# Kernel optimization log

Measured on AMD Instinct MI355X. Metric: run time of the kernel, lower is better.

Reference implementation:

```python
import jax, jax.numpy as jnp
import numpy as np

N_JOBS, N_MACH = 30, 20
N = N_JOBS * N_MACH          # 600 nodes
IN_DIM = 2
H = 128                      # hidden_dim_feature_extractor
HA = 256                     # hidden_dim_actor
HC = 256                     # hidden_dim_critic
E = 9600                     # edges
BN_EPS = 1e-5


def setup_inputs() -> dict:
    key = jax.random.key(0)
    ks = jax.random.split(key, 16)
    init = lambda k, shp: (jax.random.normal(k, shp, jnp.float32) * 0.05)
    d = {
        "features": jax.random.normal(ks[0], (N, IN_DIM), jnp.float32),
        "edge_index": jax.random.randint(ks[1], (2, E), 0, N, jnp.int32),
        # GIN layer 0 MLP: Linear(IN,H) -> BN -> ReLU -> Linear(H,H)
        "g0_W0": init(ks[2], (IN_DIM, H)), "g0_b0": jnp.zeros((H,), jnp.float32),
        "g0_gamma": jnp.ones((H,), jnp.float32), "g0_beta": jnp.zeros((H,), jnp.float32),
        "g0_W1": init(ks[3], (H, H)), "g0_b1": jnp.zeros((H,), jnp.float32),
        # GIN layer 1 MLP: Linear(H,H) -> BN -> ReLU -> Linear(H,H)
        "g1_W0": init(ks[4], (H, H)), "g1_b0": jnp.zeros((H,), jnp.float32),
        "g1_gamma": jnp.ones((H,), jnp.float32), "g1_beta": jnp.zeros((H,), jnp.float32),
        "g1_W1": init(ks[5], (H, H)), "g1_b1": jnp.zeros((H,), jnp.float32),
        # actor MLP: Linear(3H,HA) -> ReLU -> Linear(HA,1)
        "a_W0": init(ks[6], (3 * H, HA)), "a_b0": jnp.zeros((HA,), jnp.float32),
        "a_W1": init(ks[7], (HA, 1)), "a_b1": jnp.zeros((1,), jnp.float32),
        # critic MLP: Linear(H,HC) -> ReLU -> Linear(HC,1)
        "c_W0": init(ks[8], (H, HC)), "c_b0": jnp.zeros((HC,), jnp.float32),
        "c_W1": init(ks[9], (HC, 1)), "c_b1": jnp.zeros((1,), jnp.float32),
    }
    return d


def _gin_mlp(h, W0, b0, gamma, beta, W1, b1):
    # Linear -> BatchNorm(train-mode batch stats) -> ReLU -> Linear
    h1 = h @ W0 + b0
    mu = h1.mean(axis=0)
    var = h1.var(axis=0)
    h1 = gamma * (h1 - mu) * jax.lax.rsqrt(var + BN_EPS) + beta
    return jax.nn.relu(h1) @ W1 + b1


def reference(features, edge_index,
              g0_W0, g0_b0, g0_gamma, g0_beta, g0_W1, g0_b1,
              g1_W0, g1_b0, g1_gamma, g1_beta, g1_W1, g1_b1,
              a_W0, a_b0, a_W1, a_b1,
              c_W0, c_b0, c_W1, c_b1):
    src, dst = edge_index[0], edge_index[1]

    def gin(x, *mlp_params):
        # GINConv with eps=0: MLP(x + sum_{j in N(i)} x_j)
        agg = jax.ops.segment_sum(x[src], dst, num_segments=N)
        return _gin_mlp(x + agg, *mlp_params)

    h = gin(features, g0_W0, g0_b0, g0_gamma, g0_beta, g0_W1, g0_b1)
    h = gin(h, g1_W0, g1_b0, g1_gamma, g1_beta, g1_W1, g1_b1)   # (N, H)

    # graph pooling: (ones/N) @ h  == mean over nodes
    ge = h.mean(axis=0, keepdims=True)                           # (1, H)
    value = jax.nn.relu(ge @ c_W0 + c_b0) @ c_W1 + c_b1          # (1, 1)

    # s_a_pairs row k (k = i*N + j): [ge, h[j] (tile), h[i] (repeat_interleave)]
    # Fuse concat + first actor matmul by splitting a_W0 into three H-blocks.
    Ws, Wn1, Wn2 = a_W0[:H], a_W0[H:2 * H], a_W0[2 * H:]
    pre = (ge @ Ws + a_b0)[None, :, :] + (h @ Wn1)[None, :, :] + (h @ Wn2)[:, None, :]
    logits = jax.nn.relu(pre).reshape(N * N, HA) @ a_W1 + a_b1   # (N^2, 1)
    pi = jax.nn.softmax(logits, axis=0)
    return pi, value
```

## Files before the change

### kernel.cpp

```cpp
#include <hip/hip_runtime.h>
#include <math.h>

#define N_NODES 600
#define N_EDGES 9600
#define HDIM    128
#define HA      256
#define NN      360000
#define BN_EPS  1e-5f
#define NTILE   361

#define OFF_U     0
#define OFF_BAB   1200
#define OFF_SUMZ  1456
#define OFF_SUMZ2 1584
#define OFF_R1SUM 1712
#define OFF_MAXA  1840
#define OFF_SUMA  2352
#define OFF_CSR   2864
#define OFF_WC1   13072
#define OFF_WC2   45840
#define OFF_H0    78608
#define OFF_Z     155408
#define OFF_A     232208
#define OFF_B     385808

typedef _Float16 h2 __attribute__((ext_vector_type(2)));
typedef _Float16 h4 __attribute__((ext_vector_type(4)));
typedef _Float16 h8 __attribute__((ext_vector_type(8)));

__device__ __forceinline__ float dot2acc(h2 a, h2 b, float c) {
#if __has_builtin(__builtin_amdgcn_fdot2)
  return __builtin_amdgcn_fdot2(a, b, c, false);
#else
  return c + (float)a.x * (float)b.x + (float)a.y * (float)b.y;
#endif
}

__device__ __forceinline__ h2 relu2(h2 x) {
  h2 z = {(_Float16)0, (_Float16)0};
#if __has_builtin(__builtin_elementwise_max)
  return __builtin_elementwise_max(x, z);
#else
  h2 r;
  r.x = x.x > z.x ? x.x : z.x;
  r.y = x.y > z.y ? x.y : z.y;
  return r;
#endif
}

__device__ __forceinline__ h4 toh4(float4 v) {
  h4 r;
  r.x = (_Float16)v.x; r.y = (_Float16)v.y;
  r.z = (_Float16)v.z; r.w = (_Float16)v.w;
  return r;
}

struct KP {
  const float* feat; const int* ei;
  const float *g0W0, *g0ga, *g0be, *g0W1, *g0b1;
  const float *g1W0, *g1ga, *g1be, *g1W1, *g1b1;
  const float *aW0, *ab0, *aW1;
  const float *cW0, *cb0, *cW1, *cb1;
  float* ws; float* out;
};

__global__ __launch_bounds__(256) void k_indep(KP p) {
  __shared__ float sm[1536];
  const int b = blockIdx.x, t = threadIdx.x;

  if (b < 25) {
    float* us = sm;
    if (t < 48) us[t] = 0.f;
    __syncthreads();
    const int lo = b * 24, hi = lo + 24;
    for (int e = t; e < N_EDGES; e += 256) {
      int d = p.ei[N_EDGES + e];
      if (d >= lo && d < hi) {
        int s = p.ei[e];
        atomicAdd(&us[2 * (d - lo)],     p.feat[2 * s]);
        atomicAdd(&us[2 * (d - lo) + 1], p.feat[2 * s + 1]);
      }
    }
    __syncthreads();
    if (t < 48) p.ws[OFF_U + b * 48 + t] = us[t] + p.feat[b * 48 + t];
  } else if (b == 25) {
    int* si = (int*)sm;
    int* cnt = si; int* bs = si + 600; int* off = si + 856;
    int* rs_g = (int*)(p.ws + OFF_CSR);
    int* src_g = rs_g + 604;
    for (int i = t; i < 600; i += 256) cnt[i] = 0;
    __syncthreads();
    for (int e = t; e < N_EDGES; e += 256) atomicAdd(&cnt[p.ei[N_EDGES + e]], 1);
    __syncthreads();
    int lsum = 0;
    if (t < 200) lsum = cnt[3 * t] + cnt[3 * t + 1] + cnt[3 * t + 2];
    bs[t] = lsum; __syncthreads();
    for (int d = 1; d < 256; d <<= 1) {
      int v = (t >= d) ? bs[t - d] : 0;
      __syncthreads();
      bs[t] += v;
      __syncthreads();
    }
    if (t < 200) {
      int base = bs[t] - lsum;
      off[3 * t] = base;
      off[3 * t + 1] = base + cnt[3 * t];
      off[3 * t + 2] = base + cnt[3 * t] + cnt[3 * t + 1];
    }
    if (t == 0) off[600] = N_EDGES;
    __syncthreads();
    for (int i = t; i < 601; i += 256) rs_g[i] = off[i];
    for (int i = t; i < 600; i += 256) cnt[i] = off[i];
    __syncthreads();
    for (int e = t; e < N_EDGES; e += 256) {
      int d = p.ei[N_EDGES + e];
      int pos = atomicAdd(&cnt[d], 1);
      src_g[pos] = p.ei[e];
    }
  } else if (b < 90) {
    int o = (b - 26) * 1024 + t * 4;
    int mat = o >> 15, rem = o & 32767;
    int j = rem >> 8, k = rem & 255;
    const float* aw = p.aW0 + (HDIM + mat * HDIM) * HA + k;
    float4 acc = make_float4(0, 0, 0, 0);
#pragma unroll 8
    for (int m = 0; m < HDIM; m++) {
      float w = p.g1W1[j * HDIM + m];
      const float4 v = *(const float4*)(aw + m * HA);
      acc.x += w * v.x; acc.y += w * v.y; acc.z += w * v.z; acc.w += w * v.w;
    }
    *(float4*)(p.ws + (mat ? OFF_WC2 : OFF_WC1) + j * HA + k) = acc;
  } else {
    float acc = 0.f;
#pragma unroll 8
    for (int m = 0; m < HDIM; m++)
      acc += p.g1b1[m] * (p.aW0[(HDIM + m) * HA + t] + p.aW0[(2 * HDIM + m) * HA + t]);
    p.ws[OFF_BAB + t] = acc;
    if (t < 128) {
      p.ws[OFF_SUMZ + t] = 0.f;
      p.ws[OFF_SUMZ2 + t] = 0.f;
      p.ws[OFF_R1SUM + t] = 0.f;
    }
  }
}

__global__ __launch_bounds__(256) void k_l0(KP p) {
  __shared__ float ua[1200];
  __shared__ float bn[384];
  __shared__ float r0s[512];
  __shared__ float wred[24];
  const int b = blockIdx.x, t = threadIdx.x;
  for (int i = t; i < 1200; i += 256) ua[i] = p.ws[OFF_U + i];
  __syncthreads();
  float s0 = 0, s1 = 0, s00 = 0, s11 = 0, s01 = 0;
  for (int n = t; n < N_NODES; n += 256) {
    float u0 = ua[2 * n], u1 = ua[2 * n + 1];
    s0 += u0; s1 += u1; s00 += u0 * u0; s11 += u1 * u1; s01 += u0 * u1;
  }
#pragma unroll
  for (int off = 32; off > 0; off >>= 1) {
    s0  += __shfl_xor(s0, off);  s1  += __shfl_xor(s1, off);
    s00 += __shfl_xor(s00, off); s11 += __shfl_xor(s11, off);
    s01 += __shfl_xor(s01, off);
  }
  const int wv = t >> 6, ln = t & 63;
  if (ln == 0) {
    wred[wv * 5 + 0] = s0;  wred[wv * 5 + 1] = s1;  wred[wv * 5 + 2] = s00;
    wred[wv * 5 + 3] = s11; wred[wv * 5 + 4] = s01;
  }
  __syncthreads();
  if (t < HDIM) {
    float tot[5];
#pragma unroll
    for (int q = 0; q < 5; q++)
      tot[q] = wred[q] + wred[5 + q] + wred[10 + q] + wred[15 + q];
    float m0 = tot[0] / 600.f, m1 = tot[1] / 600.f;
    float v00 = tot[2] / 600.f - m0 * m0;
    float v11 = tot[3] / 600.f - m1 * m1;
    float v01 = tot[4] / 600.f - m0 * m1;
    float W00 = p.g0W0[t], W01 = p.g0W0[HDIM + t];
    float var = W00 * W00 * v00 + W01 * W01 * v11 + 2.f * W00 * W01 * v01;
    float sc = p.g0ga[t] * rsqrtf(var + BN_EPS);
    float mu = m0 * W00 + m1 * W01;
    bn[t] = sc * W00; bn[128 + t] = sc * W01; bn[256 + t] = p.g0be[t] - mu * sc;
  }
  __syncthreads();
  const int n0 = b * 4;
#pragma unroll
  for (int pq = 0; pq < 2; pq++) {
    int idx = pq * 256 + t, n = idx >> 7, j = idx & 127;
    float u0 = ua[2 * (n0 + n)], u1 = ua[2 * (n0 + n) + 1];
    r0s[n * 128 + j] = fmaxf(u0 * bn[j] + u1 * bn[128 + j] + bn[256 + j], 0.f);
  }
  __syncthreads();
#pragma unroll
  for (int pq = 0; pq < 2; pq++) {
    int idx = pq * 256 + t, n = idx >> 7, c = idx & 127;
    const float* row = r0s + n * 128;
    float acc = p.g0b1[c];
#pragma unroll 8
    for (int j = 0; j < HDIM; j++) acc += row[j] * p.g0W1[j * HDIM + c];
    p.ws[OFF_H0 + (n0 + n) * HDIM + c] = acc;
  }
}

__global__ __launch_bounds__(256) void k_zstats(KP p) {
  __shared__ float t1[4 * 128];
  __shared__ float red[256];
  const int b = blockIdx.x, t = threadIdx.x, n0 = b * 4;
  const int* rs = (const int*)(p.ws + OFF_CSR);
  const int* srcv = rs + 604;
  const float* h0 = p.ws + OFF_H0;
#pragma unroll
  for (int pq = 0; pq < 2; pq++) {
    int idx = pq * 256 + t, n = idx >> 7, c = idx & 127;
    int node = n0 + n;
    float v = h0[node * HDIM + c];
    int e0 = rs[node], e1 = rs[node + 1];
    for (int e = e0; e < e1; e++) v += h0[srcv[e] * HDIM + c];
    t1[n * 128 + c] = v;
  }
  __syncthreads();
  float zs = 0.f, zs2 = 0.f;
#pragma unroll
  for (int pq = 0; pq < 2; pq++) {
    int idx = pq * 256 + t, n = idx >> 7, c = idx & 127;
    const float* row = t1 + n * 128;
    float acc = 0.f;
#pragma unroll 8
    for (int j = 0; j < HDIM; j++) acc += row[j] * p.g1W0[j * HDIM + c];
    p.ws[OFF_Z + (n0 + n) * HDIM + c] = acc;
    zs += acc; zs2 += acc * acc;
  }
  red[t] = zs; __syncthreads();
  if (t < 128) atomicAdd(&p.ws[OFF_SUMZ + t], red[t] + red[t + 128]);
  __syncthreads();
  red[t] = zs2; __syncthreads();
  if (t < 128) atomicAdd(&p.ws[OFF_SUMZ2 + t], red[t] + red[t + 128]);
}

__global__ __launch_bounds__(256) void k_rab(KP p) {
  __shared__ float r1[4 * 128];
  __shared__ float scl[128], shf[128];
  const int b = blockIdx.x, t = threadIdx.x, n0 = b * 4;
  if (t < 128) {
    float mu = p.ws[OFF_SUMZ + t] * (1.f / 600.f);
    float var = p.ws[OFF_SUMZ2 + t] * (1.f / 600.f) - mu * mu;
    float sc = p.g1ga[t] * rsqrtf(var + BN_EPS);
    scl[t] = sc; shf[t] = p.g1be[t] - mu * sc;
  }
  __syncthreads();
#pragma unroll
  for (int pq = 0; pq < 2; pq++) {
    int idx = pq * 256 + t, n = idx >> 7, j = idx & 127;
    float z = p.ws[OFF_Z + (n0 + n) * HDIM + j];
    r1[n * 128 + j] = fmaxf(z * scl[j] + shf[j], 0.f);
  }
  __syncthreads();
  if (t < 128)
    atomicAdd(&p.ws[OFF_R1SUM + t], r1[t] + r1[128 + t] + r1[256 + t] + r1[384 + t]);
  const float* wc1 = p.ws + OFF_WC1;
  const float* wc2 = p.ws + OFF_WC2;
  float a0 = 0, a1 = 0, a2 = 0, a3 = 0, b0 = 0, b1 = 0, b2 = 0, b3 = 0;
#pragma unroll 4
  for (int j = 0; j < HDIM; j++) {
    float w1 = wc1[j * HA + t], w2 = wc2[j * HA + t];
    float r0v = r1[j], r1v = r1[128 + j], r2v = r1[256 + j], r3v = r1[384 + j];
    a0 += r0v * w1; a1 += r1v * w1; a2 += r2v * w1; a3 += r3v * w1;
    b0 += r0v * w2; b1 += r1v * w2; b2 += r2v * w2; b3 += r3v * w2;
  }
  float* A = p.ws + OFF_A; float* Bm = p.ws + OFF_B;
  A[n0 * HA + t] = a0; A[(n0 + 1) * HA + t] = a1;
  A[(n0 + 2) * HA + t] = a2; A[(n0 + 3) * HA + t] = a3;
  Bm[n0 * HA + t] = b0; Bm[(n0 + 1) * HA + t] = b1;
  Bm[(n0 + 2) * HA + t] = b2; Bm[(n0 + 3) * HA + t] = b3;
}

__global__ __launch_bounds__(256) void k_heads(KP p) {
  __shared__ h4 AsL[2048];
  __shared__ h4 BsL[2048];
  __shared__ h4 wlp[64];
  __shared__ h4 hsp[64];
  __shared__ float ge[128];
  __shared__ float geh[128];
  __shared__ float hsge[256];
  __shared__ float red[256];
  const int b = blockIdx.x, t = threadIdx.x;

  if (t < 128) ge[t] = p.ws[OFF_R1SUM + t] * (1.f / 600.f);
  __syncthreads();
  if (t < 128) {
    float acc = p.g1b1[t];
#pragma unroll 8
    for (int j = 0; j < HDIM; j++) acc += ge[j] * p.g1W1[j * HDIM + t];
    geh[t] = acc;
  }
  __syncthreads();
  {
    float acc = p.ab0[t] + p.ws[OFF_BAB + t];
#pragma unroll 8
    for (int c = 0; c < HDIM; c++) acc += geh[c] * p.aW0[c * HA + t];
    hsge[t] = acc;
  }
  if (b == 0) {
    float v = p.cb0[t];
#pragma unroll 8
    for (int c = 0; c < HDIM; c++) v += geh[c] * p.cW0[c * HA + t];
    v = fmaxf(v, 0.f);
    red[t] = v * p.cW1[t];
    __syncthreads();
    for (int off = 128; off > 0; off >>= 1) {
      if (t < off) red[t] += red[t + off];
      __syncthreads();
    }
    if (t == 0) p.out[NN] = red[0] + p.cb1[0];
  }
  __syncthreads();
  if (t < 64) {
    wlp[t] = toh4(*(const float4*)(p.aW1 + 4 * t));
    hsp[t] = toh4(*(const float4*)(hsge + 4 * t));
  }
  __syncthreads();

  const int tj = b % 19, ti = b / 19;
  const int j0 = tj * 32, i0 = ti * 32;
  const float* A  = p.ws + OFF_A;
  const float* Bm = p.ws + OFF_B;
#pragma unroll
  for (int q = 0; q < 8; q++) {
    int f = q * 256 + t;
    int r = f >> 6;
    int c4 = f & 63;
    int k = c4 * 4;
    int sw = c4 * 32 + (r ^ (c4 & 30));
    float4 av = (j0 + r < N_NODES) ? *(const float4*)(A + (j0 + r) * HA + k)
                                   : make_float4(0, 0, 0, 0);
    AsL[sw] = toh4(av) + hsp[c4];
    float4 bv = (i0 + r < N_NODES) ? *(const float4*)(Bm + (i0 + r) * HA + k)
                                   : make_float4(0, 0, 0, 0);
    BsL[sw] = toh4(bv);
  }
  __syncthreads();

  const int tx = t & 15, ty = t >> 4;
  const int jl = tx * 2, il = ty * 2;
  float a00 = 0, a01 = 0, a10 = 0, a11 = 0;
#pragma unroll 8
  for (int kk2 = 0; kk2 < 64; kk2++) {
    int s = kk2 & 30;
    h8 va = *(h8*)&AsL[kk2 * 32 + (jl ^ s)];
    h8 vb = *(h8*)&BsL[kk2 * 32 + (il ^ s)];
    h4 vw = wlp[kk2];
    h2 wlo = __builtin_shufflevector(vw, vw, 0, 1);
    h2 whi = __builtin_shufflevector(vw, vw, 2, 3);
    h2 aj0lo = __builtin_shufflevector(va, va, 0, 1);
    h2 aj0hi = __builtin_shufflevector(va, va, 2, 3);
    h2 aj1lo = __builtin_shufflevector(va, va, 4, 5);
    h2 aj1hi = __builtin_shufflevector(va, va, 6, 7);
    h2 bi0lo = __builtin_shufflevector(vb, vb, 0, 1);
    h2 bi0hi = __builtin_shufflevector(vb, vb, 2, 3);
    h2 bi1lo = __builtin_shufflevector(vb, vb, 4, 5);
    h2 bi1hi = __builtin_shufflevector(vb, vb, 6, 7);
    a00 = dot2acc(relu2(aj0lo + bi0lo), wlo, a00);
    a00 = dot2acc(relu2(aj0hi + bi0hi), whi, a00);
    a01 = dot2acc(relu2(aj1lo + bi0lo), wlo, a01);
    a01 = dot2acc(relu2(aj1hi + bi0hi), whi, a01);
    a10 = dot2acc(relu2(aj0lo + bi1lo), wlo, a10);
    a10 = dot2acc(relu2(aj0hi + bi1hi), whi, a10);
    a11 = dot2acc(relu2(aj1lo + bi1lo), wlo, a11);
    a11 = dot2acc(relu2(aj1hi + bi1hi), whi, a11);
  }

  const int gi = i0 + il, gj = j0 + jl;
  const bool vi0 = gi < N_NODES, vi1 = gi + 1 < N_NODES;
  const bool vj0 = gj < N_NODES, vj1 = gj + 1 < N_NODES;
  float m = -INFINITY;
  if (vi0 && vj0) m = fmaxf(m, a00);
  if (vi0 && vj1) m = fmaxf(m, a01);
  if (vi1 && vj0) m = fmaxf(m, a10);
  if (vi1 && vj1) m = fmaxf(m, a11);
  __syncthreads();
  red[t] = m;
  __syncthreads();
  for (int off = 128; off > 0; off >>= 1) {
    if (t < off) red[t] = fmaxf(red[t], red[t + off]);
    __syncthreads();
  }
  const float mb = red[0];
  float s = 0.f;
  if (vi0 && vj0) { float e = expf(a00 - mb); p.out[gi * N_NODES + gj] = e; s += e; }
  if (vi0 && vj1) { float e = expf(a01 - mb); p.out[gi * N_NODES + gj + 1] = e; s += e; }
  if (vi1 && vj0) { float e = expf(a10 - mb); p.out[(gi + 1) * N_NODES + gj] = e; s += e; }
  if (vi1 && vj1) { float e = expf(a11 - mb); p.out[(gi + 1) * N_NODES + gj + 1] = e; s += e; }
  __syncthreads();
  red[t] = s;
  __syncthreads();
  for (int off = 128; off > 0; off >>= 1) {
    if (t < off) red[t] += red[t + off];
    __syncthreads();
  }
  if (t == 0) { p.ws[OFF_MAXA + b] = mb; p.ws[OFF_SUMA + b] = red[0]; }
}

__global__ __launch_bounds__(256) void k_fin(KP p) {
  __shared__ float red[256];
  __shared__ float sc19[19];
  const int b = blockIdx.x, t = threadIdx.x;
  const float* maxa = p.ws + OFF_MAXA;
  const float* suma = p.ws + OFF_SUMA;
  float m = -INFINITY;
  if (t < NTILE) m = maxa[t];
  if (t + 256 < NTILE) m = fmaxf(m, maxa[t + 256]);
  red[t] = m;
  __syncthreads();
  for (int off = 128; off > 0; off >>= 1) {
    if (t < off) red[t] = fmaxf(red[t], red[t + off]);
    __syncthreads();
  }
  const float gmax = red[0];
  __syncthreads();
  float s = 0.f;
  if (t < NTILE) s += suma[t] * expf(maxa[t] - gmax);
  if (t + 256 < NTILE) s += suma[t + 256] * expf(maxa[t + 256] - gmax);
  red[t] = s;
  __syncthreads();
  for (int off = 128; off > 0; off >>= 1) {
    if (t < off) red[t] += red[t + off];
    __syncthreads();
  }
  const float invtot = 1.0f / red[0];
  const int ti = b >> 5;
  if (t < 19) sc19[t] = expf(maxa[ti * 19 + t] - gmax) * invtot;
  __syncthreads();
  if (t < 150) {
    float4 v = *(const float4*)(p.out + b * N_NODES + 4 * t);
    float sc = sc19[(4 * t) >> 5];
    v.x *= sc; v.y *= sc; v.z *= sc; v.w *= sc;
    *(float4*)(p.out + b * N_NODES + 4 * t) = v;
  }
}

extern "C" void kernel_launch(void* const* d_in, const int* in_sizes, int n_in,
                              void* d_out, int out_size, void* d_ws, size_t ws_size,
                              hipStream_t stream) {
  KP p;
  p.feat = (const float*)d_in[0];
  p.ei   = (const int*)  d_in[1];
  p.g0W0 = (const float*)d_in[2];
  p.g0ga = (const float*)d_in[4];  p.g0be = (const float*)d_in[5];
  p.g0W1 = (const float*)d_in[6];  p.g0b1 = (const float*)d_in[7];
  p.g1W0 = (const float*)d_in[8];
  p.g1ga = (const float*)d_in[10]; p.g1be = (const float*)d_in[11];
  p.g1W1 = (const float*)d_in[12]; p.g1b1 = (const float*)d_in[13];
  p.aW0  = (const float*)d_in[14]; p.ab0  = (const float*)d_in[15];
  p.aW1  = (const float*)d_in[16];
  p.cW0  = (const float*)d_in[18]; p.cb0  = (const float*)d_in[19];
  p.cW1  = (const float*)d_in[20]; p.cb1  = (const float*)d_in[21];
  p.ws   = (float*)d_ws;
  p.out  = (float*)d_out;

  k_indep <<<91,    256, 0, stream>>>(p);
  k_l0    <<<150,   256, 0, stream>>>(p);
  k_zstats<<<150,   256, 0, stream>>>(p);
  k_rab   <<<150,   256, 0, stream>>>(p);
  k_heads <<<NTILE, 256, 0, stream>>>(p);
  k_fin   <<<600,   256, 0, stream>>>(p);
}
```

Baseline: 93.34 us.

## Fold GIN layer-0 output linear into layer-1 weights and fuse kernels

Result: faster. 79.75 us (-14.6%).

```diff
diff --git a/kernel.cpp b/kernel.cpp
--- a/kernel.cpp
+++ b/kernel.cpp
@@ -5,24 +5,28 @@
 #define N_EDGES 9600
 #define HDIM    128
 #define HA      256
+#define HC      256
 #define NN      360000
 #define BN_EPS  1e-5f
 #define NTILE   361
 
-#define OFF_U     0
-#define OFF_BAB   1200
-#define OFF_SUMZ  1456
-#define OFF_SUMZ2 1584
-#define OFF_R1SUM 1712
-#define OFF_MAXA  1840
-#define OFF_SUMA  2352
-#define OFF_CSR   2864
-#define OFF_WC1   13072
-#define OFF_WC2   45840
-#define OFF_H0    78608
-#define OFF_Z     155408
-#define OFF_A     232208
-#define OFF_B     385808
+#define OFF_U      0
+#define OFF_BCONST 1200
+#define OFF_BF     1456
+#define OFF_SUMZ   1584
+#define OFF_SUMZ2  1712
+#define OFF_R1SUM  1840
+#define OFF_RACC   1968
+#define OFF_MAXA   2224
+#define OFF_SUMA   2736
+#define OFF_CSR    3248
+#define OFF_WF     13456
+#define OFF_WC1    29840
+#define OFF_WC2    62608
+#define OFF_WGS    95376
+#define OFF_Z      128144
+#define OFF_A      204944
+#define OFF_B      358544
 
 typedef _Float16 h2 __attribute__((ext_vector_type(2)));
 typedef _Float16 h4 __attribute__((ext_vector_type(4)));
@@ -117,11 +121,12 @@
       int pos = atomicAdd(&cnt[d], 1);
       src_g[pos] = p.ei[e];
     }
-  } else if (b < 90) {
+  } else if (b < 122) {
     int o = (b - 26) * 1024 + t * 4;
     int mat = o >> 15, rem = o & 32767;
     int j = rem >> 8, k = rem & 255;
-    const float* aw = p.aW0 + (HDIM + mat * HDIM) * HA + k;
+    int rowbase = (mat == 0) ? HDIM : (mat == 1 ? 2 * HDIM : 0);
+    const float* aw = p.aW0 + rowbase * HA + k;
     float4 acc = make_float4(0, 0, 0, 0);
 #pragma unroll 8
     for (int m = 0; m < HDIM; m++) {
@@ -129,14 +134,34 @@
       const float4 v = *(const float4*)(aw + m * HA);
       acc.x += w * v.x; acc.y += w * v.y; acc.z += w * v.z; acc.w += w * v.w;
     }
-    *(float4*)(p.ws + (mat ? OFF_WC2 : OFF_WC1) + j * HA + k) = acc;
+    int dst = (mat == 0) ? OFF_WC1 : (mat == 1 ? OFF_WC2 : OFF_WGS);
+    *(float4*)(p.ws + dst + j * HA + k) = acc;
+  } else if (b < 138) {
+    int o = (b - 122) * 1024 + t * 4;
+    int j = o >> 7, c = o & 127;
+    float4 acc = make_float4(0, 0, 0, 0);
+#pragma unroll 8
+    for (int m = 0; m < HDIM; m++) {
+      float w = p.g0W1[j * HDIM + m];
+      const float4 v = *(const float4*)(p.g1W0 + m * HDIM + c);
+      acc.x += w * v.x; acc.y += w * v.y; acc.z += w * v.z; acc.w += w * v.w;
+    }
+    *(float4*)(p.ws + OFF_WF + j * HDIM + c) = acc;
   } else {
     float acc = 0.f;
 #pragma unroll 8
-    for (int m = 0; m < HDIM; m++)
-      acc += p.g1b1[m] * (p.aW0[(HDIM + m) * HA + t] + p.aW0[(2 * HDIM + m) * HA + t]);
-    p.ws[OFF_BAB + t] = acc;
+    for (int m = 0; m < HDIM; m++) {
+      float gb = p.g1b1[m];
+      acc += gb * (p.aW0[m * HA + t] + p.aW0[(HDIM + m) * HA + t] +
+                   p.aW0[(2 * HDIM + m) * HA + t]);
+    }
+    p.ws[OFF_BCONST + t] = p.ab0[t] + acc;
+    p.ws[OFF_RACC + t] = 0.f;
     if (t < 128) {
+      float a2 = 0.f;
+#pragma unroll 8
+      for (int m = 0; m < HDIM; m++) a2 += p.g0b1[m] * p.g1W0[m * HDIM + t];
+      p.ws[OFF_BF + t] = a2;
       p.ws[OFF_SUMZ + t] = 0.f;
       p.ws[OFF_SUMZ2 + t] = 0.f;
       p.ws[OFF_R1SUM + t] = 0.f;
@@ -144,17 +169,19 @@
   }
 }
 
-__global__ __launch_bounds__(256) void k_l0(KP p) {
-  __shared__ float ua[1200];
+__global__ __launch_bounds__(256) void k_zagg(KP p) {
+  __shared__ float2 u2[600];
   __shared__ float bn[384];
-  __shared__ float r0s[512];
+  __shared__ float r0agg[512];
+  __shared__ float red[256];
   __shared__ float wred[24];
-  const int b = blockIdx.x, t = threadIdx.x;
-  for (int i = t; i < 1200; i += 256) ua[i] = p.ws[OFF_U + i];
+  const int b = blockIdx.x, t = threadIdx.x, n0 = b * 4;
+  const float2* ug = (const float2*)(p.ws + OFF_U);
+  for (int i = t; i < 600; i += 256) u2[i] = ug[i];
   __syncthreads();
   float s0 = 0, s1 = 0, s00 = 0, s11 = 0, s01 = 0;
   for (int n = t; n < N_NODES; n += 256) {
-    float u0 = ua[2 * n], u1 = ua[2 * n + 1];
+    float u0 = u2[n].x, u1 = u2[n].y;
     s0 += u0; s1 += u1; s00 += u0 * u0; s11 += u1 * u1; s01 += u0 * u1;
   }
 #pragma unroll
@@ -185,51 +212,34 @@
     bn[t] = sc * W00; bn[128 + t] = sc * W01; bn[256 + t] = p.g0be[t] - mu * sc;
   }
   __syncthreads();
-  const int n0 = b * 4;
-#pragma unroll
-  for (int pq = 0; pq < 2; pq++) {
-    int idx = pq * 256 + t, n = idx >> 7, j = idx & 127;
-    float u0 = ua[2 * (n0 + n)], u1 = ua[2 * (n0 + n) + 1];
-    r0s[n * 128 + j] = fmaxf(u0 * bn[j] + u1 * bn[128 + j] + bn[256 + j], 0.f);
-  }
-  __syncthreads();
-#pragma unroll
-  for (int pq = 0; pq < 2; pq++) {
-    int idx = pq * 256 + t, n = idx >> 7, c = idx & 127;
-    const float* row = r0s + n * 128;
-    float acc = p.g0b1[c];
-#pragma unroll 8
-    for (int j = 0; j < HDIM; j++) acc += row[j] * p.g0W1[j * HDIM + c];
-    p.ws[OFF_H0 + (n0 + n) * HDIM + c] = acc;
-  }
-}
-
-__global__ __launch_bounds__(256) void k_zstats(KP p) {
-  __shared__ float t1[4 * 128];
-  __shared__ float red[256];
-  const int b = blockIdx.x, t = threadIdx.x, n0 = b * 4;
   const int* rs = (const int*)(p.ws + OFF_CSR);
   const int* srcv = rs + 604;
-  const float* h0 = p.ws + OFF_H0;
 #pragma unroll
   for (int pq = 0; pq < 2; pq++) {
-    int idx = pq * 256 + t, n = idx >> 7, c = idx & 127;
-    int node = n0 + n;
-    float v = h0[node * HDIM + c];
+    int idx = pq * 256 + t, n = idx >> 7, c = idx & 127, node = n0 + n;
+    float b0c = bn[c], b1c = bn[128 + c], b2c = bn[256 + c];
+    float2 uo = u2[node];
+    float acc = fmaxf(uo.x * b0c + uo.y * b1c + b2c, 0.f);
     int e0 = rs[node], e1 = rs[node + 1];
-    for (int e = e0; e < e1; e++) v += h0[srcv[e] * HDIM + c];
-    t1[n * 128 + c] = v;
-  }
-  __syncthreads();
+    for (int e = e0; e < e1; e++) {
+      float2 us = u2[srcv[e]];
+      acc += fmaxf(us.x * b0c + us.y * b1c + b2c, 0.f);
+    }
+    r0agg[n * 128 + c] = acc;
+  }
+  __syncthreads();
+  const float* Wf = p.ws + OFF_WF;
+  const float* bf = p.ws + OFF_BF;
   float zs = 0.f, zs2 = 0.f;
 #pragma unroll
   for (int pq = 0; pq < 2; pq++) {
-    int idx = pq * 256 + t, n = idx >> 7, c = idx & 127;
-    const float* row = t1 + n * 128;
-    float acc = 0.f;
-#pragma unroll 8
-    for (int j = 0; j < HDIM; j++) acc += row[j] * p.g1W0[j * HDIM + c];
-    p.ws[OFF_Z + (n0 + n) * HDIM + c] = acc;
+    int idx = pq * 256 + t, n = idx >> 7, c = idx & 127, node = n0 + n;
+    const float* row = r0agg + n * 128;
+    int deg = rs[node + 1] - rs[node];
+    float acc = (1.f + (float)deg) * bf[c];
+#pragma unroll 8
+    for (int j = 0; j < HDIM; j++) acc += row[j] * Wf[j * HDIM + c];
+    p.ws[OFF_Z + node * HDIM + c] = acc;
     zs += acc; zs2 += acc * acc;
   }
   red[t] = zs; __syncthreads();
@@ -241,7 +251,7 @@
 
 __global__ __launch_bounds__(256) void k_rab(KP p) {
   __shared__ float r1[4 * 128];
-  __shared__ float scl[128], shf[128];
+  __shared__ float scl[128], shf[128], rsum4[128];
   const int b = blockIdx.x, t = threadIdx.x, n0 = b * 4;
   if (t < 128) {
     float mu = p.ws[OFF_SUMZ + t] * (1.f / 600.f);
@@ -257,18 +267,25 @@
     r1[n * 128 + j] = fmaxf(z * scl[j] + shf[j], 0.f);
   }
   __syncthreads();
-  if (t < 128)
-    atomicAdd(&p.ws[OFF_R1SUM + t], r1[t] + r1[128 + t] + r1[256 + t] + r1[384 + t]);
+  if (t < 128) {
+    float s = r1[t] + r1[128 + t] + r1[256 + t] + r1[384 + t];
+    rsum4[t] = s;
+    atomicAdd(&p.ws[OFF_R1SUM + t], s);
+  }
+  __syncthreads();
   const float* wc1 = p.ws + OFF_WC1;
   const float* wc2 = p.ws + OFF_WC2;
-  float a0 = 0, a1 = 0, a2 = 0, a3 = 0, b0 = 0, b1 = 0, b2 = 0, b3 = 0;
+  const float* wgs = p.ws + OFF_WGS;
+  float a0 = 0, a1 = 0, a2 = 0, a3 = 0, b0 = 0, b1 = 0, b2 = 0, b3 = 0, rc = 0;
 #pragma unroll 4
   for (int j = 0; j < HDIM; j++) {
-    float w1 = wc1[j * HA + t], w2 = wc2[j * HA + t];
+    float w1 = wc1[j * HA + t], w2 = wc2[j * HA + t], wg = wgs[j * HA + t];
     float r0v = r1[j], r1v = r1[128 + j], r2v = r1[256 + j], r3v = r1[384 + j];
     a0 += r0v * w1; a1 += r1v * w1; a2 += r2v * w1; a3 += r3v * w1;
     b0 += r0v * w2; b1 += r1v * w2; b2 += r2v * w2; b3 += r3v * w2;
-  }
+    rc += rsum4[j] * wg;
+  }
+  atomicAdd(&p.ws[OFF_RACC + t], rc);
   float* A = p.ws + OFF_A; float* Bm = p.ws + OFF_B;
   A[n0 * HA + t] = a0; A[(n0 + 1) * HA + t] = a1;
   A[(n0 + 2) * HA + t] = a2; A[(n0 + 3) * HA + t] = a3;
@@ -281,33 +298,41 @@
   __shared__ h4 BsL[2048];
   __shared__ h4 wlp[64];
   __shared__ h4 hsp[64];
+  __shared__ float hsl[256];
   __shared__ float ge[128];
   __shared__ float geh[128];
-  __shared__ float hsge[256];
   __shared__ float red[256];
   const int b = blockIdx.x, t = threadIdx.x;
 
-  if (t < 128) ge[t] = p.ws[OFF_R1SUM + t] * (1.f / 600.f);
-  __syncthreads();
-  if (t < 128) {
-    float acc = p.g1b1[t];
-#pragma unroll 8
-    for (int j = 0; j < HDIM; j++) acc += ge[j] * p.g1W1[j * HDIM + t];
-    geh[t] = acc;
-  }
-  __syncthreads();
-  {
-    float acc = p.ab0[t] + p.ws[OFF_BAB + t];
-#pragma unroll 8
-    for (int c = 0; c < HDIM; c++) acc += geh[c] * p.aW0[c * HA + t];
-    hsge[t] = acc;
-  }
+  hsl[t] = p.ws[OFF_RACC + t] * (1.f / 600.f) + p.ws[OFF_BCONST + t];
+
   if (b == 0) {
-    float v = p.cb0[t];
-#pragma unroll 8
-    for (int c = 0; c < HDIM; c++) v += geh[c] * p.cW0[c * HA + t];
-    v = fmaxf(v, 0.f);
-    red[t] = v * p.cW1[t];
+    if (t < 128) ge[t] = p.ws[OFF_R1SUM + t] * (1.f / 600.f);
+    __syncthreads();
+    if (t < 128) {
+      float a0 = p.g1b1[t], a1 = 0.f, a2 = 0.f, a3 = 0.f;
+#pragma unroll 4
+      for (int j = 0; j < HDIM; j += 4) {
+        a0 += ge[j]     * p.g1W1[(j)     * HDIM + t];
+        a1 += ge[j + 1] * p.g1W1[(j + 1) * HDIM + t];
+        a2 += ge[j + 2] * p.g1W1[(j + 2) * HDIM + t];
+        a3 += ge[j + 3] * p.g1W1[(j + 3) * HDIM + t];
+      }
+      geh[t] = (a0 + a1) + (a2 + a3);
+    }
+    __syncthreads();
+    {
+      float v0 = p.cb0[t], v1 = 0.f, v2 = 0.f, v3 = 0.f;
+#pragma unroll 4
+      for (int c = 0; c < HDIM; c += 4) {
+        v0 += geh[c]     * p.cW0[(c)     * HC + t];
+        v1 += geh[c + 1] * p.cW0[(c + 1) * HC + t];
+        v2 += geh[c + 2] * p.cW0[(c + 2) * HC + t];
+        v3 += geh[c + 3] * p.cW0[(c + 3) * HC + t];
+      }
+      float v = fmaxf((v0 + v1) + (v2 + v3), 0.f);
+      red[t] = v * p.cW1[t];
+    }
     __syncthreads();
     for (int off = 128; off > 0; off >>= 1) {
       if (t < off) red[t] += red[t + off];
@@ -318,7 +343,7 @@
   __syncthreads();
   if (t < 64) {
     wlp[t] = toh4(*(const float4*)(p.aW1 + 4 * t));
-    hsp[t] = toh4(*(const float4*)(hsge + 4 * t));
+    hsp[t] = toh4(*(const float4*)(hsl + 4 * t));
   }
   __syncthreads();
 
@@ -429,14 +454,20 @@
     __syncthreads();
   }
   const float invtot = 1.0f / red[0];
-  const int ti = b >> 5;
+  const int ti = (b * 4) >> 5;
   if (t < 19) sc19[t] = expf(maxa[ti * 19 + t] - gmax) * invtot;
   __syncthreads();
-  if (t < 150) {
-    float4 v = *(const float4*)(p.out + b * N_NODES + 4 * t);
-    float sc = sc19[(4 * t) >> 5];
-    v.x *= sc; v.y *= sc; v.z *= sc; v.w *= sc;
-    *(float4*)(p.out + b * N_NODES + 4 * t) = v;
+#pragma unroll
+  for (int pass = 0; pass < 3; pass++) {
+    int f4 = pass * 256 + t;
+    if (f4 < 600) {
+      int r = f4 / 150, c4 = (f4 % 150) * 4;
+      float* pp = p.out + (b * 4 + r) * N_NODES + c4;
+      float4 v = *(const float4*)pp;
+      float sc = sc19[c4 >> 5];
+      v.x *= sc; v.y *= sc; v.z *= sc; v.w *= sc;
+      *(float4*)pp = v;
+    }
   }
 }
 
@@ -459,10 +490,9 @@
   p.ws   = (float*)d_ws;
   p.out  = (float*)d_out;
 
-  k_indep <<<91,    256, 0, stream>>>(p);
-  k_l0    <<<150,   256, 0, stream>>>(p);
-  k_zstats<<<150,   256, 0, stream>>>(p);
-  k_rab   <<<150,   256, 0, stream>>>(p);
-  k_heads <<<NTILE, 256, 0, stream>>>(p);
-  k_fin   <<<600,   256, 0, stream>>>(p);
-}
+  k_indep<<<139,   256, 0, stream>>>(p);
+  k_zagg <<<150,   256, 0, stream>>>(p);
+  k_rab  <<<150,   256, 0, stream>>>(p);
+  k_heads<<<NTILE, 256, 0, stream>>>(p);
+  k_fin  <<<150,   256, 0, stream>>>(p);
+}
```
